# Kernel optimization log

Hardware: AMD Instinct MI355X
Metric: run time of the kernel (lower is better)

The kernel has to match this reference:

```python
import jax, jax.numpy as jnp
import numpy as np

H = 16      # query heads
G = 4       # kv heads
D = 64      # head dim
ROPE_BASE = 10000.0

def _rotate_half(t):
    t1, t2 = jnp.split(t, 2, axis=-1)
    return jnp.concatenate([-t2, t1], axis=-1)

def _rope_emb(n):
    inv_freq = 1.0 / (ROPE_BASE ** (jnp.arange(0, D, 2, dtype=jnp.float32) / D))
    freqs = jnp.outer(jnp.arange(n, dtype=jnp.float32), inv_freq)  # [n, D/2]
    return jnp.concatenate([freqs, freqs], axis=-1)               # [n, D]

def setup_inputs() -> dict:
    key = jax.random.key(0)
    k1, k2, k3, k4 = jax.random.split(key, 4)
    B, N, C = 2, 2048, 1024
    x = jax.random.normal(k1, (B, N, C), dtype=jnp.float32)
    w_q = jax.random.normal(k2, (C, C), dtype=jnp.float32) * 0.02
    w_kv = jax.random.normal(k3, (C, 2 * G * D), dtype=jnp.float32) * 0.02
    w_out = jax.random.normal(k4, (C, C), dtype=jnp.float32) * 0.02
    return {"x": x, "w_q": w_q, "w_kv": w_kv, "w_out": w_out}

def reference(x, w_q, w_kv, w_out):
    B, N, C = x.shape
    scale = D ** -0.5
    q = (x @ w_q).reshape(B, N, H, D).transpose(0, 2, 1, 3)        # [B,H,N,D]
    kv = x @ w_kv
    k, v = jnp.split(kv, 2, axis=-1)
    k = k.reshape(B, N, G, D).transpose(0, 2, 1, 3)                # [B,G,N,D]
    v = v.reshape(B, N, G, D).transpose(0, 2, 1, 3)
    emb = _rope_emb(N)                                             # [N,D]
    cos, sin = jnp.cos(emb), jnp.sin(emb)
    q = q * cos + _rotate_half(q) * sin
    k = k * cos + _rotate_half(k) * sin
    # NOTE: faithful to source einsum -- kv-head axis g is SUMMED (absent from output)
    scores = jnp.einsum('bhid,bgjd->bhij', q, k) * scale           # [B,H,N,N]
    probs = jax.nn.softmax(scores, axis=-1)
    out = jnp.einsum('bhij,bgjd->bhid', probs, v)                  # [B,H,N,D]
    out = out.transpose(0, 2, 1, 3).reshape(B, N, H * D)
    return out @ w_out
```

## Files before the change

### kernel.cpp

```cpp
#include <hip/hip_runtime.h>
#include <hip/hip_bf16.h>
#include <math.h>

#define B_ 2
#define N_ 2048
#define C_ 1024
#define H_ 16
#define G_ 4
#define D_ 64
#define QKV_N 1152

using short8  = __attribute__((ext_vector_type(8))) short;
using short4v = __attribute__((ext_vector_type(4))) short;
using float4v = __attribute__((ext_vector_type(4))) float;

#if __has_builtin(__builtin_amdgcn_mfma_f32_16x16x16_bf16)
#define MFMA16K16(A, B, C) __builtin_amdgcn_mfma_f32_16x16x16_bf16(A, B, C, 0, 0, 0)
#else
#define MFMA16K16(A, B, C) __builtin_amdgcn_mfma_f32_16x16x16bf16_1k(A, B, C, 0, 0, 0)
#endif

__device__ __forceinline__ ushort f2bf(float f) {
    union { float f; unsigned u; } v; v.f = f;
    unsigned r = (v.u + 0x7FFF + ((v.u >> 16) & 1)) >> 16;
    return (ushort)r;
}
__device__ __forceinline__ float bf2f(ushort u) {
    union { unsigned u; float f; } t; t.u = ((unsigned)u) << 16; return t.f;
}
__device__ __forceinline__ unsigned pack_bf16(float a, float b) {
#if __has_builtin(__builtin_amdgcn_cvt_pk_bf16_f32)
    auto t = __builtin_amdgcn_cvt_pk_bf16_f32(a, b);
    unsigned r; __builtin_memcpy(&r, &t, 4); return r;
#else
    return (unsigned)f2bf(a) | ((unsigned)f2bf(b) << 16);
#endif
}
__device__ __forceinline__ float fexp2(float x) {
#if __has_builtin(__builtin_amdgcn_exp2f)
    return __builtin_amdgcn_exp2f(x);
#else
    return exp2f(x);
#endif
}

__device__ void tconv_body(const float* __restrict__ src, ushort* __restrict__ dst,
                           int K, int N, int bx, int by, float (*T)[65]) {
    const int n0 = bx * 64, k0 = by * 64;
    const int tid = threadIdx.x;
    #pragma unroll
    for (int s = 0; s < 16; ++s) {
        int idx = tid + s * 256; int r = idx >> 6, cc = idx & 63;
        T[r][cc] = src[(size_t)(k0 + r) * N + n0 + cc];
    }
    __syncthreads();
    #pragma unroll
    for (int s = 0; s < 16; ++s) {
        int idx = tid + s * 256; int r = idx >> 6, cc = idx & 63;
        dst[(size_t)(n0 + r) * K + k0 + cc] = f2bf(T[cc][r]);
    }
}

__global__ void prep(const float* __restrict__ x, const float* __restrict__ w_q,
                     const float* __restrict__ w_kv, const float* __restrict__ w_out,
                     ushort* __restrict__ xb, ushort* __restrict__ wqkvT,
                     ushort* __restrict__ woutT) {
    __shared__ float T[64][65];
    const int blk = blockIdx.x, tid = threadIdx.x;
    if (blk < 4096) {
        int i = blk * 1024 + tid * 4;
        float4 v = *(const float4*)(x + i);
        ushort4 o;
        o.x = f2bf(v.x); o.y = f2bf(v.y); o.z = f2bf(v.z); o.w = f2bf(v.w);
        *(ushort4*)(xb + i) = o;
    } else if (blk < 4352) {
        int idx = blk - 4096;
        tconv_body(w_q, wqkvT, C_, C_, idx & 15, idx >> 4, T);
    } else if (blk < 4608) {
        int idx = blk - 4352;
        tconv_body(w_out, woutT, C_, C_, idx & 15, idx >> 4, T);
    } else {
        const int k0 = (blk - 4608) * 64;
        #pragma unroll
        for (int it = 0; it < 4; ++it) {
            int p = tid + it * 256;
            int kk = p >> 4, d4 = (p & 15) * 4;
            float ks[4] = {0, 0, 0, 0}, vs[4] = {0, 0, 0, 0};
            #pragma unroll
            for (int g = 0; g < G_; ++g) {
                float4 a = *(const float4*)(w_kv + (size_t)(k0 + kk) * 512 + g * 64 + d4);
                float4 b = *(const float4*)(w_kv + (size_t)(k0 + kk) * 512 + 256 + g * 64 + d4);
                ks[0] += a.x; ks[1] += a.y; ks[2] += a.z; ks[3] += a.w;
                vs[0] += b.x; vs[1] += b.y; vs[2] += b.z; vs[3] += b.w;
            }
            #pragma unroll
            for (int e = 0; e < 4; ++e) {
                wqkvT[(size_t)(1024 + d4 + e) * C_ + k0 + kk] = f2bf(ks[e]);
                wqkvT[(size_t)(1088 + d4 + e) * C_ + k0 + kk] = f2bf(vs[e]);
            }
        }
    }
}

template <int MODE>
__global__ __launch_bounds__(256) void gemm128p(const ushort* __restrict__ A,
                                                const ushort* __restrict__ Bt,
                                                void* __restrict__ Cv,
                                                ushort* __restrict__ Kt,
                                                ushort* __restrict__ VtT,
                                                int M, int N, int K) {
    __shared__ __align__(16) ushort As[2][128 * 64];
    __shared__ __align__(16) ushort Bs[2][64 * 64];

    const int tid = threadIdx.x, wave = tid >> 6, lane = tid & 63;
    const int g = lane >> 4, c = lane & 15;
    const int m0 = blockIdx.y * 128, n0 = blockIdx.x * 64;

    const int lr = tid >> 3;
    const int lq = tid & 7;
    const int gsw = (lq ^ (lr & 7)) * 8;
    const ushort* pa = A  + (size_t)(m0 + lr) * K + gsw;
    const ushort* pb = Bt + (size_t)(n0 + lr) * K + gsw;

    auto stage = [&](int buf, int k0) {
        #pragma unroll
        for (int i = 0; i < 4; ++i)
            __builtin_amdgcn_global_load_lds(
                (const __attribute__((address_space(1))) void*)(pa + (size_t)i * 32 * K + k0),
                (__attribute__((address_space(3))) void*)&As[buf][(i * 32 + wave * 8) * 64], 16, 0, 0);
        #pragma unroll
        for (int i = 0; i < 2; ++i)
            __builtin_amdgcn_global_load_lds(
                (const __attribute__((address_space(1))) void*)(pb + (size_t)i * 32 * K + k0),
                (__attribute__((address_space(3))) void*)&Bs[buf][(i * 32 + wave * 8) * 64], 16, 0, 0);
    };

    float4v acc[2][4];
    #pragma unroll
    for (int m = 0; m < 2; ++m)
        #pragma unroll
        for (int n = 0; n < 4; ++n) acc[m][n] = {0, 0, 0, 0};

    stage(0, 0);
    __syncthreads();

    const int NT = K >> 6;
    int cur = 0;
    for (int t = 0; t < NT; ++t) {
        if (t + 1 < NT) stage(cur ^ 1, (t + 1) << 6);

        #pragma unroll
        for (int kk = 0; kk < 2; ++kk) {
            const int c7 = c & 7;
            short8 af[2], bf[4];
            #pragma unroll
            for (int m = 0; m < 2; ++m)
                af[m] = *(const short8*)&As[cur][(wave * 32 + m * 16 + c) * 64 + ((kk * 4 + g) ^ c7) * 8];
            #pragma unroll
            for (int n = 0; n < 4; ++n)
                bf[n] = *(const short8*)&Bs[cur][(n * 16 + c) * 64 + ((kk * 4 + g) ^ c7) * 8];
            #pragma unroll
            for (int m = 0; m < 2; ++m)
                #pragma unroll
                for (int n = 0; n < 4; ++n)
                    acc[m][n] = __builtin_amdgcn_mfma_f32_16x16x32_bf16(af[m], bf[n], acc[m][n], 0, 0, 0);
        }
        __syncthreads();
        cur ^= 1;
    }

    if (MODE == 1 && blockIdx.x >= 16) {
        if (blockIdx.x == 16) {
            const float invf_e = __powf(10000.0f, -(float)c * (1.0f / 32.0f));
            const float invf_o = __powf(10000.0f, -(float)(c + 16) * (1.0f / 32.0f));
            #pragma unroll
            for (int m = 0; m < 2; ++m)
                #pragma unroll
                for (int r = 0; r < 4; ++r) {
                    const int rowi = m0 + wave * 32 + m * 16 + 4 * g + r;
                    const float nf = (float)(rowi & (N_ - 1));
                    float sn0, cs0, sn1, cs1;
                    __sincosf(nf * invf_e, &sn0, &cs0);
                    __sincosf(nf * invf_o, &sn1, &cs1);
                    #pragma unroll
                    for (int nn = 0; nn < 4; ++nn) {
                        const float v = acc[m][nn][r], p = acc[m][nn ^ 2][r];
                        const float rh = (nn < 2) ? -p : p;
                        const float sn = (nn & 1) ? sn1 : sn0;
                        const float cs = (nn & 1) ? cs1 : cs0;
                        Kt[(size_t)rowi * 64 + nn * 16 + c] = f2bf(v * cs + rh * sn);
                    }
                }
        } else {
            #pragma unroll
            for (int m = 0; m < 2; ++m)
                #pragma unroll
                for (int nn = 0; nn < 4; ++nn)
                    #pragma unroll
                    for (int r = 0; r < 4; ++r) {
                        const int rowi = m0 + wave * 32 + m * 16 + 4 * g + r;
                        const int n = rowi & (N_ - 1), bb = rowi >> 11;
                        VtT[((size_t)bb * 64 + nn * 16 + c) * N_ + n] = f2bf(acc[m][nn][r]);
                    }
        }
        return;
    }

    #pragma unroll
    for (int m = 0; m < 2; ++m)
        #pragma unroll
        for (int n = 0; n < 4; ++n)
            #pragma unroll
            for (int r = 0; r < 4; ++r) {
                int rowi = m0 + wave * 32 + m * 16 + 4 * g + r;
                int coli = n0 + n * 16 + c;
                if (MODE == 2) ((float*)Cv)[(size_t)rowi * N + coli] = acc[m][n][r];
                else ((ushort*)Cv)[(size_t)rowi * N + coli] = f2bf(acc[m][n][r]);
            }
}

#define QSCALE 0.18033688011112042f

__global__ __launch_bounds__(256) void attn13(
        const ushort* __restrict__ qkvb, const ushort* __restrict__ Kt,
        const ushort* __restrict__ VtT,
        ushort* __restrict__ oP0, ushort* __restrict__ oP1,
        ushort* __restrict__ oP2, ushort* __restrict__ oP3,
        float* __restrict__ lP) {
    const int s  = blockIdx.x & 3;
    const int qt = (blockIdx.x >> 2) & 7;
    const int h  = (blockIdx.x >> 5) & 15;
    const int b  = blockIdx.x >> 9;
    const int tid = threadIdx.x, wave = tid >> 6, lane = tid & 63;
    const int g = lane >> 4, c = lane & 15;

    __shared__ __align__(16) ushort Ksh[64 * 64];
    __shared__ __align__(16) ushort Vsh[64 * 64];

    ushort* oPs = (s == 0) ? oP0 : (s == 1) ? oP1 : (s == 2) ? oP2 : oP3;

    const int i0 = qt * 256 + wave * 64;
    float invf[8];
    #pragma unroll
    for (int i = 0; i < 8; ++i)
        invf[i] = __powf(10000.0f, -(float)(8 * g + i) * (1.0f / 32.0f));

    short8 qf[4][2];
    #pragma unroll
    for (int a = 0; a < 4; ++a) {
        const int row = i0 + a * 16 + c;
        const ushort* qrow = qkvb + (size_t)(b * N_ + row) * QKV_N + h * 64;
        short8 raw0 = *(const short8*)(qrow + 8 * g);
        short8 raw1 = *(const short8*)(qrow + 32 + 8 * g);
        #pragma unroll
        for (int i = 0; i < 8; ++i) {
            float f0 = bf2f((ushort)raw0[i]), f1 = bf2f((ushort)raw1[i]);
            float sn, cs; __sincosf((float)row * invf[i], &sn, &cs);
            qf[a][0][i] = (short)f2bf((f0 * cs - f1 * sn) * QSCALE);
            qf[a][1][i] = (short)f2bf((f1 * cs + f0 * sn) * QSCALE);
        }
    }

    float4v o[4][4];
    #pragma unroll
    for (int a = 0; a < 4; ++a)
        #pragma unroll
        for (int f = 0; f < 4; ++f) o[a][f] = {0, 0, 0, 0};
    float ll[4] = {0.f, 0.f, 0.f, 0.f};

    const ushort* Kb = Kt  + (size_t)b * N_ * 64;
    const ushort* Vb = VtT + (size_t)b * 64 * N_;
    const int lr8 = lane >> 3, lq8 = lane & 7;
    const int wpos = (lq8 ^ lr8) * 8;
    const int j0 = s * (N_ / 4);
    const int NT = (N_ / 4) / 64;

    short8 kr0 = *(const short8*)(Kb + (size_t)(j0 + wave * 16 + lr8) * 64 + lq8 * 8);
    short8 kr1 = *(const short8*)(Kb + (size_t)(j0 + wave * 16 + 8 + lr8) * 64 + lq8 * 8);
    short8 vr0 = *(const short8*)(Vb + (size_t)(wave * 16 + lr8) * N_ + j0 + lq8 * 8);
    short8 vr1 = *(const short8*)(Vb + (size_t)(wave * 16 + 8 + lr8) * N_ + j0 + lq8 * 8);

    for (int t = 0; t < NT; ++t) {
        __syncthreads();
        *(short8*)&Ksh[(wave * 16 + lr8) * 64 + wpos]     = kr0;
        *(short8*)&Ksh[(wave * 16 + 8 + lr8) * 64 + wpos] = kr1;
        *(short8*)&Vsh[(wave * 16 + lr8) * 64 + wpos]     = vr0;
        *(short8*)&Vsh[(wave * 16 + 8 + lr8) * 64 + wpos] = vr1;
        __syncthreads();
        if (t + 1 < NT) {
            const int jn = j0 + (t + 1) * 64;
            kr0 = *(const short8*)(Kb + (size_t)(jn + wave * 16 + lr8) * 64 + lq8 * 8);
            kr1 = *(const short8*)(Kb + (size_t)(jn + wave * 16 + 8 + lr8) * 64 + lq8 * 8);
            vr0 = *(const short8*)(Vb + (size_t)(wave * 16 + lr8) * N_ + jn + lq8 * 8);
            vr1 = *(const short8*)(Vb + (size_t)(wave * 16 + 8 + lr8) * N_ + jn + lq8 * 8);
        }

        #pragma unroll
        for (int jt4 = 0; jt4 < 4; ++jt4) {
            const int R = jt4 * 16 + c;
            short8 kf0 = *(const short8*)&Ksh[R * 64 + ((g ^ (c & 7)) * 8)];
            short8 kf1 = *(const short8*)&Ksh[R * 64 + (((g ^ 4) ^ (c & 7)) * 8)];
            short4v vf[4];
            #pragma unroll
            for (int f = 0; f < 4; ++f)
                vf[f] = *(const short4v*)&Vsh[(16 * f + c) * 64 +
                          (((jt4 * 2 + (g >> 1)) ^ (c & 7)) * 8) + (g & 1) * 4];

            #pragma unroll
            for (int a = 0; a < 4; ++a) {
                float4v st = {0, 0, 0, 0};
                st = __builtin_amdgcn_mfma_f32_16x16x32_bf16(kf0, qf[a][0], st, 0, 0, 0);
                st = __builtin_amdgcn_mfma_f32_16x16x32_bf16(kf1, qf[a][1], st, 0, 0, 0);
                float p0 = fexp2(st[0]), p1 = fexp2(st[1]);
                float p2 = fexp2(st[2]), p3 = fexp2(st[3]);
                ll[a] += (p0 + p1) + (p2 + p3);
                union { unsigned u[2]; short4v v; } pk;
                pk.u[0] = pack_bf16(p0, p1);
                pk.u[1] = pack_bf16(p2, p3);
                #pragma unroll
                for (int f = 0; f < 4; ++f)
                    o[a][f] = MFMA16K16(vf[f], pk.v, o[a][f]);
            }
        }
    }

    #pragma unroll
    for (int a = 0; a < 4; ++a) {
        float lt = ll[a];
        lt += __shfl_xor(lt, 16, 64);
        lt += __shfl_xor(lt, 32, 64);
        const int row = i0 + a * 16 + c;
        if (g == 0) lP[((size_t)s * (B_ * N_) + b * N_ + row) * 16 + h] = lt;
        #pragma unroll
        for (int f = 0; f < 4; ++f) {
            ushort4 w;
            w.x = f2bf(o[a][f][0]); w.y = f2bf(o[a][f][1]);
            w.z = f2bf(o[a][f][2]); w.w = f2bf(o[a][f][3]);
            *(ushort4*)(oPs + (size_t)(b * N_ + row) * 1024 + h * 64 + 16 * f + 4 * g) = w;
        }
    }
}

__global__ void combine4(const ushort* __restrict__ oP0, const ushort* __restrict__ oP1,
                         const ushort* __restrict__ oP2, const ushort* __restrict__ oP3,
                         const float* __restrict__ lP, ushort* __restrict__ ao) {
    const int e = (blockIdx.x * 256 + threadIdx.x) * 4;
    const int row = e >> 10, hh = (e >> 6) & 15;
    const size_t MH = (size_t)B_ * N_ * 16;
    const float inv = 1.0f / (lP[row * 16 + hh] + lP[MH + row * 16 + hh] +
                              lP[2 * MH + row * 16 + hh] + lP[3 * MH + row * 16 + hh]);
    ushort4 a = *(const ushort4*)(oP0 + e);
    ushort4 b = *(const ushort4*)(oP1 + e);
    ushort4 cc = *(const ushort4*)(oP2 + e);
    ushort4 d = *(const ushort4*)(oP3 + e);
    ushort4 r;
    r.x = f2bf((bf2f(a.x) + bf2f(b.x) + bf2f(cc.x) + bf2f(d.x)) * inv);
    r.y = f2bf((bf2f(a.y) + bf2f(b.y) + bf2f(cc.y) + bf2f(d.y)) * inv);
    r.z = f2bf((bf2f(a.z) + bf2f(b.z) + bf2f(cc.z) + bf2f(d.z)) * inv);
    r.w = f2bf((bf2f(a.w) + bf2f(b.w) + bf2f(cc.w) + bf2f(d.w)) * inv);
    *(ushort4*)(ao + e) = r;
}

extern "C" void kernel_launch(void* const* d_in, const int* in_sizes, int n_in,
                              void* d_out, int out_size, void* d_ws, size_t ws_size,
                              hipStream_t stream) {
    const float* x     = (const float*)d_in[0];
    const float* w_q   = (const float*)d_in[1];
    const float* w_kv  = (const float*)d_in[2];
    const float* w_out = (const float*)d_in[3];
    float* out = (float*)d_out;

    const int M = B_ * N_;
    ushort* xb    = (ushort*)d_ws;
    ushort* wqkvT = xb    + (size_t)M * C_;
    ushort* woutT = wqkvT + (size_t)QKV_N * C_;
    ushort* qkvb  = woutT + (size_t)C_ * C_;
    ushort* Kt    = qkvb  + (size_t)M * QKV_N;
    ushort* VtT   = Kt    + (size_t)B_ * N_ * D_;
    ushort* oP1   = VtT   + (size_t)B_ * D_ * N_;
    ushort* oP2   = oP1   + (size_t)M * C_;
    ushort* oP3   = oP2   + (size_t)M * C_;
    float*  lP    = (float*)(oP3 + (size_t)M * C_);
    ushort* oP0   = xb;
    ushort* ao    = xb;

    prep<<<4624, 256, 0, stream>>>(x, w_q, w_kv, w_out, xb, wqkvT, woutT);
    gemm128p<1><<<dim3(QKV_N / 64, M / 128), 256, 0, stream>>>(xb, wqkvT, qkvb, Kt, VtT, M, QKV_N, C_);
    attn13<<<B_ * H_ * (N_ / 256) * 4, 256, 0, stream>>>(qkvb, Kt, VtT, oP0, oP1, oP2, oP3, lP);
    combine4<<<(M * C_) / 1024, 256, 0, stream>>>(oP0, oP1, oP2, oP3, lP, ao);
    gemm128p<2><<<dim3(C_ / 64, M / 128), 256, 0, stream>>>(ao, woutT, out, nullptr, nullptr, M, C_, C_);
}
```

Measured before the change: 189.0 us.

## Fuse Q RoPE and scaling into QKV GEMM epilogue; split KV range in two

Q rotary embedding and the softmax scale move from the attention kernel's prologue into the QKV GEMM epilogue, so the attention kernel loads pre-rotated Q straight into registers. The attention split-K factor drops from 4 to 2, which halves the partial output buffers and the combine kernel's reads. Each attention block now does twice the KV iterations and the grid has half as many blocks (512), so there is less parallelism to hide latency. Removing two partial buffers also shrinks workspace traffic.

```diff
diff --git a/kernel.cpp b/kernel.cpp
--- a/kernel.cpp
+++ b/kernel.cpp
@@ -9,6 +9,8 @@
 #define G_ 4
 #define D_ 64
 #define QKV_N 1152
+
+#define QSCALE 0.18033688011112042f
 
 using short8  = __attribute__((ext_vector_type(8))) short;
 using short4v = __attribute__((ext_vector_type(4))) short;
@@ -169,7 +171,31 @@
         cur ^= 1;
     }
 
-    if (MODE == 1 && blockIdx.x >= 16) {
+    if (MODE == 1) {
+        if (blockIdx.x < 16) {
+            const float invf_e = __powf(10000.0f, -(float)c * (1.0f / 32.0f));
+            const float invf_o = __powf(10000.0f, -(float)(c + 16) * (1.0f / 32.0f));
+            #pragma unroll
+            for (int m = 0; m < 2; ++m)
+                #pragma unroll
+                for (int r = 0; r < 4; ++r) {
+                    const int rowi = m0 + wave * 32 + m * 16 + 4 * g + r;
+                    const float nf = (float)(rowi & (N_ - 1));
+                    float sn0, cs0, sn1, cs1;
+                    __sincosf(nf * invf_e, &sn0, &cs0);
+                    __sincosf(nf * invf_o, &sn1, &cs1);
+                    #pragma unroll
+                    for (int nn = 0; nn < 4; ++nn) {
+                        const float v = acc[m][nn][r], p = acc[m][nn ^ 2][r];
+                        const float rh = (nn < 2) ? -p : p;
+                        const float sn = (nn & 1) ? sn1 : sn0;
+                        const float cs = (nn & 1) ? cs1 : cs0;
+                        ((ushort*)Cv)[(size_t)rowi * N + n0 + nn * 16 + c] =
+                            f2bf((v * cs + rh * sn) * QSCALE);
+                    }
+                }
+            return;
+        }
         if (blockIdx.x == 16) {
             const float invf_e = __powf(10000.0f, -(float)c * (1.0f / 32.0f));
             const float invf_o = __powf(10000.0f, -(float)(c + 16) * (1.0f / 32.0f));
@@ -214,51 +240,37 @@
             for (int r = 0; r < 4; ++r) {
                 int rowi = m0 + wave * 32 + m * 16 + 4 * g + r;
                 int coli = n0 + n * 16 + c;
-                if (MODE == 2) ((float*)Cv)[(size_t)rowi * N + coli] = acc[m][n][r];
-                else ((ushort*)Cv)[(size_t)rowi * N + coli] = f2bf(acc[m][n][r]);
+                ((float*)Cv)[(size_t)rowi * N + coli] = acc[m][n][r];
             }
 }
 
-#define QSCALE 0.18033688011112042f
-
-__global__ __launch_bounds__(256) void attn13(
+__global__ __launch_bounds__(256) void attn14(
         const ushort* __restrict__ qkvb, const ushort* __restrict__ Kt,
         const ushort* __restrict__ VtT,
         ushort* __restrict__ oP0, ushort* __restrict__ oP1,
-        ushort* __restrict__ oP2, ushort* __restrict__ oP3,
-        float* __restrict__ lP) {
-    const int s  = blockIdx.x & 3;
-    const int qt = (blockIdx.x >> 2) & 7;
-    const int h  = (blockIdx.x >> 5) & 15;
-    const int b  = blockIdx.x >> 9;
+        float* __restrict__ lP0, float* __restrict__ lP1) {
+    const int s  = blockIdx.x & 1;
+    const int qt = (blockIdx.x >> 1) & 7;
+    const int h  = (blockIdx.x >> 4) & 15;
+    const int b  = blockIdx.x >> 8;
     const int tid = threadIdx.x, wave = tid >> 6, lane = tid & 63;
     const int g = lane >> 4, c = lane & 15;
 
     __shared__ __align__(16) ushort Ksh[64 * 64];
     __shared__ __align__(16) ushort Vsh[64 * 64];
 
-    ushort* oPs = (s == 0) ? oP0 : (s == 1) ? oP1 : (s == 2) ? oP2 : oP3;
+    ushort* oPs = s ? oP1 : oP0;
+    float*  lPs = s ? lP1 : lP0;
 
     const int i0 = qt * 256 + wave * 64;
-    float invf[8];
-    #pragma unroll
-    for (int i = 0; i < 8; ++i)
-        invf[i] = __powf(10000.0f, -(float)(8 * g + i) * (1.0f / 32.0f));
 
     short8 qf[4][2];
     #pragma unroll
     for (int a = 0; a < 4; ++a) {
         const int row = i0 + a * 16 + c;
         const ushort* qrow = qkvb + (size_t)(b * N_ + row) * QKV_N + h * 64;
-        short8 raw0 = *(const short8*)(qrow + 8 * g);
-        short8 raw1 = *(const short8*)(qrow + 32 + 8 * g);
-        #pragma unroll
-        for (int i = 0; i < 8; ++i) {
-            float f0 = bf2f((ushort)raw0[i]), f1 = bf2f((ushort)raw1[i]);
-            float sn, cs; __sincosf((float)row * invf[i], &sn, &cs);
-            qf[a][0][i] = (short)f2bf((f0 * cs - f1 * sn) * QSCALE);
-            qf[a][1][i] = (short)f2bf((f1 * cs + f0 * sn) * QSCALE);
-        }
+        qf[a][0] = *(const short8*)(qrow + 8 * g);
+        qf[a][1] = *(const short8*)(qrow + 32 + 8 * g);
     }
 
     float4v o[4][4];
@@ -272,8 +284,8 @@
     const ushort* Vb = VtT + (size_t)b * 64 * N_;
     const int lr8 = lane >> 3, lq8 = lane & 7;
     const int wpos = (lq8 ^ lr8) * 8;
-    const int j0 = s * (N_ / 4);
-    const int NT = (N_ / 4) / 64;
+    const int j0 = s * (N_ / 2);
+    const int NT = (N_ / 2) / 64;
 
     short8 kr0 = *(const short8*)(Kb + (size_t)(j0 + wave * 16 + lr8) * 64 + lq8 * 8);
     short8 kr1 = *(const short8*)(Kb + (size_t)(j0 + wave * 16 + 8 + lr8) * 64 + lq8 * 8);
@@ -330,7 +342,7 @@
         lt += __shfl_xor(lt, 16, 64);
         lt += __shfl_xor(lt, 32, 64);
         const int row = i0 + a * 16 + c;
-        if (g == 0) lP[((size_t)s * (B_ * N_) + b * N_ + row) * 16 + h] = lt;
+        if (g == 0) lPs[(size_t)(b * N_ + row) * 16 + h] = lt;
         #pragma unroll
         for (int f = 0; f < 4; ++f) {
             ushort4 w;
@@ -341,23 +353,19 @@
     }
 }
 
-__global__ void combine4(const ushort* __restrict__ oP0, const ushort* __restrict__ oP1,
-                         const ushort* __restrict__ oP2, const ushort* __restrict__ oP3,
-                         const float* __restrict__ lP, ushort* __restrict__ ao) {
+__global__ void combine(const ushort* __restrict__ oP0, const ushort* __restrict__ oP1,
+                        const float* __restrict__ lP0, const float* __restrict__ lP1,
+                        ushort* __restrict__ ao) {
     const int e = (blockIdx.x * 256 + threadIdx.x) * 4;
     const int row = e >> 10, hh = (e >> 6) & 15;
-    const size_t MH = (size_t)B_ * N_ * 16;
-    const float inv = 1.0f / (lP[row * 16 + hh] + lP[MH + row * 16 + hh] +
-                              lP[2 * MH + row * 16 + hh] + lP[3 * MH + row * 16 + hh]);
+    const float inv = 1.0f / (lP0[row * 16 + hh] + lP1[row * 16 + hh]);
     ushort4 a = *(const ushort4*)(oP0 + e);
     ushort4 b = *(const ushort4*)(oP1 + e);
-    ushort4 cc = *(const ushort4*)(oP2 + e);
-    ushort4 d = *(const ushort4*)(oP3 + e);
     ushort4 r;
-    r.x = f2bf((bf2f(a.x) + bf2f(b.x) + bf2f(cc.x) + bf2f(d.x)) * inv);
-    r.y = f2bf((bf2f(a.y) + bf2f(b.y) + bf2f(cc.y) + bf2f(d.y)) * inv);
-    r.z = f2bf((bf2f(a.z) + bf2f(b.z) + bf2f(cc.z) + bf2f(d.z)) * inv);
-    r.w = f2bf((bf2f(a.w) + bf2f(b.w) + bf2f(cc.w) + bf2f(d.w)) * inv);
+    r.x = f2bf((bf2f(a.x) + bf2f(b.x)) * inv);
+    r.y = f2bf((bf2f(a.y) + bf2f(b.y)) * inv);
+    r.z = f2bf((bf2f(a.z) + bf2f(b.z)) * inv);
+    r.w = f2bf((bf2f(a.w) + bf2f(b.w)) * inv);
     *(ushort4*)(ao + e) = r;
 }
 
@@ -378,15 +386,14 @@
     ushort* Kt    = qkvb  + (size_t)M * QKV_N;
     ushort* VtT   = Kt    + (size_t)B_ * N_ * D_;
     ushort* oP1   = VtT   + (size_t)B_ * D_ * N_;
-    ushort* oP2   = oP1   + (size_t)M * C_;
-    ushort* oP3   = oP2   + (size_t)M * C_;
-    float*  lP    = (float*)(oP3 + (size_t)M * C_);
+    float*  lP0   = (float*)(oP1 + (size_t)M * C_);
+    float*  lP1   = lP0 + (size_t)M * H_;
     ushort* oP0   = xb;
     ushort* ao    = xb;
 
     prep<<<4624, 256, 0, stream>>>(x, w_q, w_kv, w_out, xb, wqkvT, woutT);
     gemm128p<1><<<dim3(QKV_N / 64, M / 128), 256, 0, stream>>>(xb, wqkvT, qkvb, Kt, VtT, M, QKV_N, C_);
-    attn13<<<B_ * H_ * (N_ / 256) * 4, 256, 0, stream>>>(qkvb, Kt, VtT, oP0, oP1, oP2, oP3, lP);
-    combine4<<<(M * C_) / 1024, 256, 0, stream>>>(oP0, oP1, oP2, oP3, lP, ao);
+    attn14<<<B_ * H_ * (N_ / 256) * 2, 256, 0, stream>>>(qkvb, Kt, VtT, oP0, oP1, lP0, lP1);
+    combine<<<(M * C_) / 1024, 256, 0, stream>>>(oP0, oP1, lP0, lP1, ao);
     gemm128p<2><<<dim3(C_ / 64, M / 128), 256, 0, stream>>>(ao, woutT, out, nullptr, nullptr, M, C_, C_);
 }
```

Result: faster. 175.4 us (-7.2%).
